# Optimization experiments

Measured on AMD Instinct MI355X. Metric: run time of the kernel, lower is better.

The kernel has to match this reference:

```python
import jax, jax.numpy as jnp
import numpy as np

N, IN_DIM, L, K, D = 131072, 128, 16, 8, 50
ENC_H, DEC_H, HEAD_H, DF = 64, 16, 64, 1.0


def setup_inputs() -> dict:
    key = jax.random.key(0)
    ks = jax.random.split(key, 20)
    s = lambda k, shape, fan: jax.random.normal(k, shape, jnp.float32) * (1.0 / np.sqrt(fan))
    return {
        "x": jax.random.normal(ks[0], (N, IN_DIM), jnp.float32),
        # encoder: in -> 64 -> 64 -> L
        "We1": s(ks[1], (IN_DIM, ENC_H), IN_DIM), "be1": jnp.zeros((ENC_H,), jnp.float32),
        "We2": s(ks[2], (ENC_H, ENC_H), ENC_H),   "be2": jnp.zeros((ENC_H,), jnp.float32),
        "We3": s(ks[3], (ENC_H, L), ENC_H),       "be3": jnp.zeros((L,), jnp.float32),
        # decoder: L -> 16 -> in
        "Wd1": s(ks[4], (L, DEC_H), L),           "bd1": jnp.zeros((DEC_H,), jnp.float32),
        "Wd2": s(ks[5], (DEC_H, IN_DIM), DEC_H),  "bd2": jnp.zeros((IN_DIM,), jnp.float32),
        # K per-cluster survival heads: (L+in) -> 64 -> num_durations
        "Wh1": s(ks[6], (K, L + IN_DIM, HEAD_H), L + IN_DIM), "bh1": jnp.zeros((K, HEAD_H), jnp.float32),
        "Wh2": s(ks[7], (K, HEAD_H, D), HEAD_H),              "bh2": jnp.zeros((K, D), jnp.float32),
        # cluster centers buffer
        "centers": jax.random.normal(ks[8], (K, L), jnp.float32) * 0.05,
    }


def _student_t_sim(z, centers, df):
    # z: [N, L], centers: [K, L] -> q: [N, K]
    dist2 = jnp.sum((z[:, None, :] - centers[None, :, :]) ** 2, axis=-1)
    logits = -0.5 * (df + 1.0) * jnp.log1p(dist2 / df)
    return jax.nn.softmax(logits, axis=1)


def reference(x, We1, be1, We2, be2, We3, be3, Wd1, bd1, Wd2, bd2,
              Wh1, bh1, Wh2, bh2, centers):
    relu = jax.nn.relu
    # encoder (eval mode: dropout off, non-variational)
    e = relu(x @ We1 + be1)
    e = relu(e @ We2 + be2)
    z = e @ We3 + be3                      # [N, L]
    q = _student_t_sim(z, centers, DF)     # [N, K]
    h = jnp.concatenate([z, x], axis=1)    # [N, L+in]
    # cluster-argmax routing to per-cluster heads: compute all K, select winner
    cluster_idx = jnp.argmax(q, axis=1)    # [N]
    h1 = relu(jnp.einsum("nf,kfh->nkh", h, Wh1) + bh1[None])   # [N, K, H]
    lg = jnp.einsum("nkh,khd->nkd", h1, Wh2) + bh2[None]       # [N, K, D]
    surv_logits = jnp.take_along_axis(lg, cluster_idx[:, None, None], axis=1)[:, 0]  # [N, D]
    # decoder + reconstruction loss per sample
    d = relu(z @ Wd1 + bd1)
    x_hat = d @ Wd2 + bd2                  # [N, in]
    rec_ps = jnp.mean((x_hat - x) ** 2, axis=1)
    kld = jnp.zeros((x.shape[0],), x.dtype)
    return z, q, surv_logits, x_hat, rec_ps, kld
```

## Files before the change

### kernel.cpp

```cpp
#include <hip/hip_runtime.h>

#define NS 131072
#define KC 8
typedef unsigned long long u64;

#define LD4(P) (*reinterpret_cast<const float4*>(&sm[(P)]))
#define LD2(P) (*reinterpret_cast<const float2*>(&sm[(P)]))
#define ST4(P) (*reinterpret_cast<float4*>(&sm[(P)]))
#define ST2(P) (*reinterpret_cast<float2*>(&sm[(P)]))

#define FMA8(ACCR, AV, W0, W1) do { \
  ACCR[0]=fmaf((AV),(W0).x,ACCR[0]); ACCR[1]=fmaf((AV),(W0).y,ACCR[1]); \
  ACCR[2]=fmaf((AV),(W0).z,ACCR[2]); ACCR[3]=fmaf((AV),(W0).w,ACCR[3]); \
  ACCR[4]=fmaf((AV),(W1).x,ACCR[4]); ACCR[5]=fmaf((AV),(W1).y,ACCR[5]); \
  ACCR[6]=fmaf((AV),(W1).z,ACCR[6]); ACCR[7]=fmaf((AV),(W1).w,ACCR[7]); } while(0)

#define K4(ACC, ABASE, ASTR, AK, BBASE, BSTR, JOFF, BK) do { \
  const float4 b00=LD4((BBASE)+((BK)*4+0)*(BSTR)+(JOFF)), b01=LD4((BBASE)+((BK)*4+0)*(BSTR)+(JOFF)+4); \
  const float4 b10=LD4((BBASE)+((BK)*4+1)*(BSTR)+(JOFF)), b11=LD4((BBASE)+((BK)*4+1)*(BSTR)+(JOFF)+4); \
  const float4 b20=LD4((BBASE)+((BK)*4+2)*(BSTR)+(JOFF)), b21=LD4((BBASE)+((BK)*4+2)*(BSTR)+(JOFF)+4); \
  const float4 b30=LD4((BBASE)+((BK)*4+3)*(BSTR)+(JOFF)), b31=LD4((BBASE)+((BK)*4+3)*(BSTR)+(JOFF)+4); \
  _Pragma("unroll") \
  for (int m_ = 0; m_ < 8; ++m_) { \
    const float4 av = LD4((ABASE)+(st+32*m_)*(ASTR)+(AK)*4); \
    FMA8(ACC[m_], av.x, b00, b01); FMA8(ACC[m_], av.y, b10, b11); \
    FMA8(ACC[m_], av.z, b20, b21); FMA8(ACC[m_], av.w, b30, b31); } \
} while(0)

#define INIT88(ACC, BPTR, OFF) do { \
  const float4 u_ = *reinterpret_cast<const float4*>(&(BPTR)[(OFF)]); \
  const float4 v_ = *reinterpret_cast<const float4*>(&(BPTR)[(OFF)+4]); \
  _Pragma("unroll") for (int m_ = 0; m_ < 8; ++m_) { \
    ACC[m_][0]=u_.x; ACC[m_][1]=u_.y; ACC[m_][2]=u_.z; ACC[m_][3]=u_.w; \
    ACC[m_][4]=v_.x; ACC[m_][5]=v_.y; ACC[m_][6]=v_.z; ACC[m_][7]=v_.w; } \
} while(0)

#define RELU88(ACC) do { _Pragma("unroll") for (int m_=0;m_<8;++m_) \
  { _Pragma("unroll") for (int j_=0;j_<8;++j_) ACC[m_][j_]=fmaxf(ACC[m_][j_],0.f); } } while(0)

#define WRITE_E(ACC) do { _Pragma("unroll") for (int m_=0;m_<8;++m_){ \
  const int r_ = st + 32*m_; \
  ST4(AR + r_*72 + job)     = make_float4(ACC[m_][0],ACC[m_][1],ACC[m_][2],ACC[m_][3]); \
  ST4(AR + r_*72 + job + 4) = make_float4(ACC[m_][4],ACC[m_][5],ACC[m_][6],ACC[m_][7]); } } while(0)

#define AR  0
#define WB  18432
#define WD1 19520
#define SMW 19776

__global__ __launch_bounds__(256, 2) void k_enc(
    const float* __restrict__ x,
    const float* __restrict__ We1, const float* __restrict__ be1,
    const float* __restrict__ We2, const float* __restrict__ be2,
    const float* __restrict__ We3, const float* __restrict__ be3,
    const float* __restrict__ Wd1, const float* __restrict__ bd1,
    const float* __restrict__ Wd2, const float* __restrict__ bd2,
    const float* __restrict__ centers,
    float* __restrict__ out_z, float* __restrict__ out_q,
    float* __restrict__ xhat, float* __restrict__ rec, float* __restrict__ kld,
    int* __restrict__ cidx, int* __restrict__ counts)
{
    __shared__ float sm[SMW];
    const int t  = threadIdx.x;
    const int ot = t & 7, st = t >> 3;
    const int job = ot * 8;
    const int s0 = blockIdx.x * 256;

    {
        float acc1[8][8];
        INIT88(acc1, be1, job);
        #pragma unroll 1
        for (int c = 0; c < 8; ++c) {
            #pragma unroll
            for (int p = 0; p < 4; ++p) {
                const int g = p*256 + t, row = g >> 2, c4 = (g & 3) * 4;
                ST4(AR + row*20 + c4) = *reinterpret_cast<const float4*>(
                    &x[(size_t)(s0+row)*128 + c*16 + c4]);
            }
            {   const int row = t >> 4, c4 = (t & 15) * 4;
                ST4(WB + row*68 + c4) = *reinterpret_cast<const float4*>(
                    &We1[(size_t)(c*16 + row)*64 + c4]); }
            __syncthreads();
            #pragma unroll
            for (int kc = 0; kc < 4; ++kc) K4(acc1, AR, 20, kc, WB, 68, job, kc);
            __syncthreads();
        }
        RELU88(acc1);
        WRITE_E(acc1);
    }
    __syncthreads();

    {
        float acc2[8][8];
        INIT88(acc2, be2, job);
        #pragma unroll 1
        for (int c = 0; c < 4; ++c) {
            {   const int row = t >> 4, c4 = (t & 15) * 4;
                ST4(WB + row*68 + c4) = *reinterpret_cast<const float4*>(
                    &We2[(size_t)(c*16 + row)*64 + c4]); }
            __syncthreads();
            #pragma unroll
            for (int kc = 0; kc < 4; ++kc) K4(acc2, AR, 72, c*4 + kc, WB, 68, job, kc);
            __syncthreads();
        }
        RELU88(acc2);
        WRITE_E(acc2);
    }
    {   const int row = t >> 2, c4 = (t & 3) * 4;
        ST4(WB + row*16 + c4) = *reinterpret_cast<const float4*>(
            &We3[(size_t)row*16 + c4]); }
    if (t < 64) ST4(WD1 + (t >> 2)*16 + (t & 3)*4) =
        *reinterpret_cast<const float4*>(&Wd1[(t >> 2)*16 + (t & 3)*4]);
    __syncthreads();

    float zac[8][2];
    {   const float2 b3 = *reinterpret_cast<const float2*>(&be3[ot*2]);
        #pragma unroll
        for (int m = 0; m < 8; ++m) { zac[m][0] = b3.x; zac[m][1] = b3.y; } }
    #pragma unroll 2
    for (int kc = 0; kc < 16; ++kc) {
        const float2 w0 = LD2(WB + (kc*4+0)*16 + ot*2);
        const float2 w1 = LD2(WB + (kc*4+1)*16 + ot*2);
        const float2 w2 = LD2(WB + (kc*4+2)*16 + ot*2);
        const float2 w3 = LD2(WB + (kc*4+3)*16 + ot*2);
        #pragma unroll
        for (int m = 0; m < 8; ++m) {
            const float4 av = LD4(AR + (st + 32*m)*72 + kc*4);
            float sa = zac[m][0], sb = zac[m][1];
            sa = fmaf(av.x, w0.x, sa); sb = fmaf(av.x, w0.y, sb);
            sa = fmaf(av.y, w1.x, sa); sb = fmaf(av.y, w1.y, sb);
            sa = fmaf(av.z, w2.x, sa); sb = fmaf(av.z, w2.y, sb);
            sa = fmaf(av.w, w3.x, sa); sb = fmaf(av.w, w3.y, sb);
            zac[m][0] = sa; zac[m][1] = sb;
        }
    }
    #pragma unroll
    for (int m = 0; m < 8; ++m)
        *reinterpret_cast<float2*>(&out_z[(size_t)(s0 + st + 32*m)*16 + ot*2]) =
            make_float2(zac[m][0], zac[m][1]);
    __syncthreads();
    #pragma unroll
    for (int m = 0; m < 8; ++m)
        ST2(AR + (st + 32*m)*20 + ot*2) = make_float2(zac[m][0], zac[m][1]);
    {
        const int row = t >> 4, c4 = (t & 15) * 4;
        ST4(WB + row*68 + c4) = *reinterpret_cast<const float4*>(
            &Wd2[(size_t)row*128 + c4]); }
    __syncthreads();

    {
        const float4 z0 = LD4(AR + t*20 + 0), z1 = LD4(AR + t*20 + 4);
        const float4 z2 = LD4(AR + t*20 + 8), z3 = LD4(AR + t*20 + 12);
        const float zz[16] = {z0.x,z0.y,z0.z,z0.w, z1.x,z1.y,z1.z,z1.w,
                              z2.x,z2.y,z2.z,z2.w, z3.x,z3.y,z3.z,z3.w};
        float d2[KC];
        #pragma unroll
        for (int k = 0; k < KC; ++k) {
            float acc = 0.f;
            #pragma unroll
            for (int l = 0; l < 16; ++l) {
                const float dl = zz[l] - centers[k*16 + l];
                acc = fmaf(dl, dl, acc);
            }
            d2[k] = acc;
        }
        float lgt[KC], ex[KC];
        float mm = -1e30f;
        #pragma unroll
        for (int k = 0; k < KC; ++k) { lgt[k] = -log1pf(d2[k]); mm = fmaxf(mm, lgt[k]); }
        float ssum = 0.f;
        #pragma unroll
        for (int k = 0; k < KC; ++k) { ex[k] = expf(lgt[k] - mm); ssum += ex[k]; }
        const float inv = 1.f / ssum;
        float4* oq = reinterpret_cast<float4*>(&out_q[(size_t)(s0 + t)*8]);
        oq[0] = make_float4(ex[0]*inv, ex[1]*inv, ex[2]*inv, ex[3]*inv);
        oq[1] = make_float4(ex[4]*inv, ex[5]*inv, ex[6]*inv, ex[7]*inv);
        int ci = 0; float best = d2[0];
        #pragma unroll
        for (int k = 1; k < KC; ++k) if (d2[k] < best) { best = d2[k]; ci = k; }
        cidx[s0 + t] = ci;
        #pragma unroll
        for (int k = 0; k < KC; ++k) {
            const u64 mk = __ballot(ci == k);
            if ((t & 63) == 0 && mk) atomicAdd(&counts[k], (int)__popcll(mk));
        }
        kld[s0 + t] = 0.f;
    }

    {
        float dac[8][2];
        const float2 bb = *reinterpret_cast<const float2*>(&bd1[ot*2]);
        const float2 u0 = LD2(WD1 + 0*16 + ot*2),  u1 = LD2(WD1 + 1*16 + ot*2);
        const float2 u2 = LD2(WD1 + 2*16 + ot*2),  u3 = LD2(WD1 + 3*16 + ot*2);
        const float2 u4 = LD2(WD1 + 4*16 + ot*2),  u5 = LD2(WD1 + 5*16 + ot*2);
        const float2 u6 = LD2(WD1 + 6*16 + ot*2),  u7 = LD2(WD1 + 7*16 + ot*2);
        const float2 u8 = LD2(WD1 + 8*16 + ot*2),  u9 = LD2(WD1 + 9*16 + ot*2);
        const float2 uA = LD2(WD1 + 10*16 + ot*2), uB = LD2(WD1 + 11*16 + ot*2);
        const float2 uC = LD2(WD1 + 12*16 + ot*2), uD = LD2(WD1 + 13*16 + ot*2);
        const float2 uE = LD2(WD1 + 14*16 + ot*2), uF = LD2(WD1 + 15*16 + ot*2);
        #pragma unroll
        for (int m = 0; m < 8; ++m) {
            const int r = st + 32*m;
            const float4 a0 = LD4(AR + r*20 + 0), a1 = LD4(AR + r*20 + 4);
            const float4 a2 = LD4(AR + r*20 + 8), a3 = LD4(AR + r*20 + 12);
            float sa = bb.x, sb = bb.y;
            sa=fmaf(a0.x,u0.x,sa); sb=fmaf(a0.x,u0.y,sb);
            sa=fmaf(a0.y,u1.x,sa); sb=fmaf(a0.y,u1.y,sb);
            sa=fmaf(a0.z,u2.x,sa); sb=fmaf(a0.z,u2.y,sb);
            sa=fmaf(a0.w,u3.x,sa); sb=fmaf(a0.w,u3.y,sb);
            sa=fmaf(a1.x,u4.x,sa); sb=fmaf(a1.x,u4.y,sb);
            sa=fmaf(a1.y,u5.x,sa); sb=fmaf(a1.y,u5.y,sb);
            sa=fmaf(a1.z,u6.x,sa); sb=fmaf(a1.z,u6.y,sb);
            sa=fmaf(a1.w,u7.x,sa); sb=fmaf(a1.w,u7.y,sb);
            sa=fmaf(a2.x,u8.x,sa); sb=fmaf(a2.x,u8.y,sb);
            sa=fmaf(a2.y,u9.x,sa); sb=fmaf(a2.y,u9.y,sb);
            sa=fmaf(a2.z,uA.x,sa); sb=fmaf(a2.z,uA.y,sb);
            sa=fmaf(a2.w,uB.x,sa); sb=fmaf(a2.w,uB.y,sb);
            sa=fmaf(a3.x,uC.x,sa); sb=fmaf(a3.x,uC.y,sb);
            sa=fmaf(a3.y,uD.x,sa); sb=fmaf(a3.y,uD.y,sb);
            sa=fmaf(a3.z,uE.x,sa); sb=fmaf(a3.z,uE.y,sb);
            sa=fmaf(a3.w,uF.x,sa); sb=fmaf(a3.w,uF.y,sb);
            dac[m][0] = fmaxf(sa, 0.f); dac[m][1] = fmaxf(sb, 0.f);
        }
        __syncthreads();
        #pragma unroll
        for (int m = 0; m < 8; ++m)
            ST2(AR + (st + 32*m)*20 + ot*2) = make_float2(dac[m][0], dac[m][1]);
    }
    __syncthreads();

    float rp[8] = {0.f,0.f,0.f,0.f,0.f,0.f,0.f,0.f};
    {
        float accx[8][8];
        INIT88(accx, bd2, job);
        #pragma unroll
        for (int kc = 0; kc < 4; ++kc) K4(accx, AR, 20, kc, WB, 68, job, kc);
        #pragma unroll
        for (int m = 0; m < 8; ++m) {
            const int r = st + 32*m;
            const float4 xa = *reinterpret_cast<const float4*>(&x[(size_t)(s0+r)*128 + job]);
            const float4 xb = *reinterpret_cast<const float4*>(&x[(size_t)(s0+r)*128 + job + 4]);
            float df;
            df=accx[m][0]-xa.x; rp[m]=fmaf(df,df,rp[m]);
            df=accx[m][1]-xa.y; rp[m]=fmaf(df,df,rp[m]);
            df=accx[m][2]-xa.z; rp[m]=fmaf(df,df,rp[m]);
            df=accx[m][3]-xa.w; rp[m]=fmaf(df,df,rp[m]);
            df=accx[m][4]-xb.x; rp[m]=fmaf(df,df,rp[m]);
            df=accx[m][5]-xb.y; rp[m]=fmaf(df,df,rp[m]);
            df=accx[m][6]-xb.z; rp[m]=fmaf(df,df,rp[m]);
            df=accx[m][7]-xb.w; rp[m]=fmaf(df,df,rp[m]);
            float4* o = reinterpret_cast<float4*>(&xhat[(size_t)(s0+r)*128 + job]);
            o[0] = make_float4(accx[m][0],accx[m][1],accx[m][2],accx[m][3]);
            o[1] = make_float4(accx[m][4],accx[m][5],accx[m][6],accx[m][7]);
        }
    }
    __syncthreads();
    {   const int row = t >> 4, c4 = (t & 15) * 4;
        ST4(WB + row*68 + c4) = *reinterpret_cast<const float4*>(
            &Wd2[(size_t)row*128 + 64 + c4]); }
    __syncthreads();
    {
        float accx[8][8];
        INIT88(accx, bd2, 64 + job);
        #pragma unroll
        for (int kc = 0; kc < 4; ++kc) K4(accx, AR, 20, kc, WB, 68, job, kc);
        #pragma unroll
        for (int m = 0; m < 8; ++m) {
            const int r = st + 32*m;
            const float4 xa = *reinterpret_cast<const float4*>(&x[(size_t)(s0+r)*128 + 64 + job]);
            const float4 xb = *reinterpret_cast<const float4*>(&x[(size_t)(s0+r)*128 + 64 + job + 4]);
            float df;
            df=accx[m][0]-xa.x; rp[m]=fmaf(df,df,rp[m]);
            df=accx[m][1]-xa.y; rp[m]=fmaf(df,df,rp[m]);
            df=accx[m][2]-xa.z; rp[m]=fmaf(df,df,rp[m]);
            df=accx[m][3]-xa.w; rp[m]=fmaf(df,df,rp[m]);
            df=accx[m][4]-xb.x; rp[m]=fmaf(df,df,rp[m]);
            df=accx[m][5]-xb.y; rp[m]=fmaf(df,df,rp[m]);
            df=accx[m][6]-xb.z; rp[m]=fmaf(df,df,rp[m]);
            df=accx[m][7]-xb.w; rp[m]=fmaf(df,df,rp[m]);
            float4* o = reinterpret_cast<float4*>(&xhat[(size_t)(s0+r)*128 + 64 + job]);
            o[0] = make_float4(accx[m][0],accx[m][1],accx[m][2],accx[m][3]);
            o[1] = make_float4(accx[m][4],accx[m][5],accx[m][6],accx[m][7]);
        }
    }
    #pragma unroll
    for (int m = 0; m < 8; ++m) {
        float v = rp[m];
        v += __shfl_xor(v, 1); v += __shfl_xor(v, 2); v += __shfl_xor(v, 4);
        if (ot == 0) rec[s0 + st + 32*m] = v * (1.f/128.f);
    }
}

__global__ void k_scan(const int* __restrict__ counts,
                       int* __restrict__ bases, int* __restrict__ cursors)
{
    if (threadIdx.x == 0) {
        int acc = 0;
        for (int k = 0; k < KC; ++k) { bases[k] = acc; cursors[k] = acc; acc += counts[k]; }
    }
}

__global__ __launch_bounds__(256) void k_scatter(
    const int* __restrict__ cidx, int* __restrict__ cursors, int* __restrict__ seg)
{
    const int s = blockIdx.x * 256 + threadIdx.x;
    const int lane = threadIdx.x & 63;
    const int ci = cidx[s];
    #pragma unroll
    for (int k = 0; k < KC; ++k) {
        const u64 mk = __ballot(ci == k);
        if (ci == k) {
            const int leader = __ffsll(mk) - 1;
            int base = 0;
            if (lane == leader) base = atomicAdd(&cursors[k], (int)__popcll(mk));
            base = __shfl(base, leader, 64);
            seg[base + (int)__popcll(mk & (((u64)1 << lane) - 1))] = s;
        }
    }
}

#define SMH 19520

__global__ __launch_bounds__(256, 2) void k_heads(
    const float* __restrict__ x, const float* __restrict__ zread,
    const float* __restrict__ Wh1, const float* __restrict__ bh1,
    const float* __restrict__ Wh2, const float* __restrict__ bh2,
    const int* __restrict__ counts, const int* __restrict__ bases,
    const int* __restrict__ seg,
    float* __restrict__ surv)
{
    __shared__ float sm[SMH];
    __shared__ int idxs[256];
    const int t  = threadIdx.x;
    const int ot = t & 7, st = t >> 3;
    const int job = ot * 8;

    int kk = -1, chunk = 0, pref = 0;
    #pragma unroll
    for (int q = 0; q < KC; ++q) {
        const int ck = (counts[q] + 255) >> 8;
        if (kk < 0) {
            if ((int)blockIdx.x < pref + ck) { kk = q; chunk = (int)blockIdx.x - pref; }
            pref += ck;
        }
    }
    if (kk < 0) return;
    kk    = __builtin_amdgcn_readfirstlane(kk);
    chunk = __builtin_amdgcn_readfirstlane(chunk);
    const int cnt  = __builtin_amdgcn_readfirstlane(counts[kk]);
    const int base = __builtin_amdgcn_readfirstlane(bases[kk]);

    {   const int i = chunk*256 + t;
        idxs[t] = seg[base + ((i < cnt) ? i : (cnt - 1))]; }
    __syncthreads();

    {
        float acc1[8][8];
        INIT88(acc1, bh1, (size_t)kk*64 + job);
        #pragma unroll
        for (int p = 0; p < 4; ++p) {
            const int g = p*256 + t, row = g >> 2, c4 = (g & 3) * 4;
            ST4(AR + row*20 + c4) = *reinterpret_cast<const float4*>(
                &zread[(size_t)idxs[row]*16 + c4]);
        }
        {   const int row = t >> 4, c4 = (t & 15) * 4;
            ST4(WB + row*68 + c4) = *reinterpret_cast<const float4*>(
                &Wh1[((size_t)kk*144 + row)*64 + c4]); }
        __syncthreads();
        #pragma unroll
        for (int kc = 0; kc < 4; ++kc) K4(acc1, AR, 20, kc, WB, 68, job, kc);
        __syncthreads();
        #pragma unroll 1
        for (int c = 0; c < 8; ++c) {
            #pragma unroll
            for (int p = 0; p < 4; ++p) {
                const int g = p*256 + t, row = g >> 2, c4 = (g & 3) * 4;
                ST4(AR + row*20 + c4) = *reinterpret_cast<const float4*>(
                    &x[(size_t)idxs[row]*128 + c*16 + c4]);
            }
            {   const int row = t >> 4, c4 = (t & 15) * 4;
                ST4(WB + row*68 + c4) = *reinterpret_cast<const float4*>(
                    &Wh1[((size_t)kk*144 + 16 + c*16 + row)*64 + c4]); }
            __syncthreads();
            #pragma unroll
            for (int kc = 0; kc < 4; ++kc) K4(acc1, AR, 20, kc, WB, 68, job, kc);
            __syncthreads();
        }
        RELU88(acc1);
        WRITE_E(acc1);
    }
    __syncthreads();

    float acc2[8][8];
    {   float bz[8];
        #pragma unroll
        for (int j = 0; j < 8; ++j) {
            const int col = job + j;
            bz[j] = (col < 50) ? bh2[(size_t)kk*50 + col] : 0.f;
        }
        #pragma unroll
        for (int m = 0; m < 8; ++m) {
            #pragma unroll
            for (int j = 0; j < 8; ++j) acc2[m][j] = bz[j];
        } }
    #pragma unroll 1
    for (int c = 0; c < 4; ++c) {
        {   const int row = t >> 4, c0 = (t & 15) * 4;
            const int gk = c*16 + row;
            float4 v;
            v.x = (c0+0 < 50) ? Wh2[((size_t)kk*64 + gk)*50 + c0+0] : 0.f;
            v.y = (c0+1 < 50) ? Wh2[((size_t)kk*64 + gk)*50 + c0+1] : 0.f;
            v.z = (c0+2 < 50) ? Wh2[((size_t)kk*64 + gk)*50 + c0+2] : 0.f;
            v.w = (c0+3 < 50) ? Wh2[((size_t)kk*64 + gk)*50 + c0+3] : 0.f;
            ST4(WB + row*68 + c0) = v; }
        __syncthreads();
        #pragma unroll
        for (int kc = 0; kc < 4; ++kc) K4(acc2, AR, 72, c*4 + kc, WB, 68, job, kc);
        __syncthreads();
    }

    #pragma unroll
    for (int m = 0; m < 8; ++m) {
        const int r = st + 32*m;
        if (chunk*256 + r < cnt) {
            float* so = &surv[(size_t)idxs[r]*50 + job];
            if (ot < 6) {
                *reinterpret_cast<float2*>(&so[0]) = make_float2(acc2[m][0], acc2[m][1]);
                *reinterpret_cast<float2*>(&so[2]) = make_float2(acc2[m][2], acc2[m][3]);
                *reinterpret_cast<float2*>(&so[4]) = make_float2(acc2[m][4], acc2[m][5]);
                *reinterpret_cast<float2*>(&so[6]) = make_float2(acc2[m][6], acc2[m][7]);
            } else if (ot == 6) {
                *reinterpret_cast<float2*>(&so[0]) = make_float2(acc2[m][0], acc2[m][1]);
            }
        }
    }
}

extern "C" void kernel_launch(void* const* d_in, const int* in_sizes, int n_in,
                              void* d_out, int out_size, void* d_ws, size_t ws_size,
                              hipStream_t stream)
{
    const float* x   = (const float*)d_in[0];
    const float* We1 = (const float*)d_in[1];
    const float* be1 = (const float*)d_in[2];
    const float* We2 = (const float*)d_in[3];
    const float* be2 = (const float*)d_in[4];
    const float* We3 = (const float*)d_in[5];
    const float* be3 = (const float*)d_in[6];
    const float* Wd1 = (const float*)d_in[7];
    const float* bd1 = (const float*)d_in[8];
    const float* Wd2 = (const float*)d_in[9];
    const float* bd2 = (const float*)d_in[10];
    const float* Wh1 = (const float*)d_in[11];
    const float* bh1 = (const float*)d_in[12];
    const float* Wh2 = (const float*)d_in[13];
    const float* bh2 = (const float*)d_in[14];
    const float* cen = (const float*)d_in[15];
    float* out = (float*)d_out;

    float* out_z  = out;
    float* out_q  = out + (size_t)NS * 16;
    float* out_sv = out + (size_t)NS * 24;
    float* out_xh = out + (size_t)NS * 74;
    float* out_rc = out + (size_t)NS * 202;
    float* out_kl = out + (size_t)NS * 203;

    int* cidx    = (int*)d_ws;
    int* counts  = cidx + NS;
    int* bases   = counts + KC;
    int* cursors = bases + KC;
    int* seg     = cursors + KC;

    hipMemsetAsync(counts, 0, KC * sizeof(int), stream);

    k_enc<<<dim3(NS / 256), dim3(256), 0, stream>>>(
        x, We1, be1, We2, be2, We3, be3, Wd1, bd1, Wd2, bd2, cen,
        out_z, out_q, out_xh, out_rc, out_kl, cidx, counts);

    k_scan<<<dim3(1), dim3(64), 0, stream>>>(counts, bases, cursors);

    k_scatter<<<dim3(NS / 256), dim3(256), 0, stream>>>(cidx, cursors, seg);

    k_heads<<<dim3(NS / 256 + KC), dim3(256), 0, stream>>>(
        x, out_z, Wh1, bh1, Wh2, bh2, counts, bases, seg, out_sv);
}
```

Baseline: 497.3 us.

## Prefetch next x/weight chunks into registers during FMA loops

The encoder and head GEMM loops now load the next chunk of x and the weights into registers before computing on the current chunk, so global load latency overlaps the FMAs instead of stalling behind a barrier. The activation row stride in shared memory drops from 72 to 68 floats, which shrinks the LDS footprint. Launch bounds change from 2 to 1 blocks per SM, allowing more registers per thread to hold the prefetch buffers. The risk is lower occupancy, which could expose latency elsewhere, and a possible change in LDS bank conflicts from the new stride.

Result: no change. 501.6 us (+0.9%).

```diff
diff --git a/kernel.cpp b/kernel.cpp
--- a/kernel.cpp
+++ b/kernel.cpp
@@ -8,6 +8,7 @@
 #define LD2(P) (*reinterpret_cast<const float2*>(&sm[(P)]))
 #define ST4(P) (*reinterpret_cast<float4*>(&sm[(P)]))
 #define ST2(P) (*reinterpret_cast<float2*>(&sm[(P)]))
+#define GL4(P) (*reinterpret_cast<const float4*>(&(P)))
 
 #define FMA8(ACCR, AV, W0, W1) do { \
   ACCR[0]=fmaf((AV),(W0).x,ACCR[0]); ACCR[1]=fmaf((AV),(W0).y,ACCR[1]); \
@@ -40,15 +41,21 @@
 
 #define WRITE_E(ACC) do { _Pragma("unroll") for (int m_=0;m_<8;++m_){ \
   const int r_ = st + 32*m_; \
-  ST4(AR + r_*72 + job)     = make_float4(ACC[m_][0],ACC[m_][1],ACC[m_][2],ACC[m_][3]); \
-  ST4(AR + r_*72 + job + 4) = make_float4(ACC[m_][4],ACC[m_][5],ACC[m_][6],ACC[m_][7]); } } while(0)
+  ST4(AR + r_*68 + job)     = make_float4(ACC[m_][0],ACC[m_][1],ACC[m_][2],ACC[m_][3]); \
+  ST4(AR + r_*68 + job + 4) = make_float4(ACC[m_][4],ACC[m_][5],ACC[m_][6],ACC[m_][7]); } } while(0)
+
+#define STAGE_X() do { \
+  ST4(AR + (xr0      )*20 + xc) = rx0; \
+  ST4(AR + (xr0 +  64)*20 + xc) = rx1; \
+  ST4(AR + (xr0 + 128)*20 + xc) = rx2; \
+  ST4(AR + (xr0 + 192)*20 + xc) = rx3; } while(0)
 
 #define AR  0
-#define WB  18432
-#define WD1 19520
-#define SMW 19776
-
-__global__ __launch_bounds__(256, 2) void k_enc(
+#define WB  17408
+#define WD1 18496
+#define SMW 18752
+
+__global__ __launch_bounds__(256, 1) void k_enc(
     const float* __restrict__ x,
     const float* __restrict__ We1, const float* __restrict__ be1,
     const float* __restrict__ We2, const float* __restrict__ be2,
@@ -65,52 +72,59 @@
     const int ot = t & 7, st = t >> 3;
     const int job = ot * 8;
     const int s0 = blockIdx.x * 256;
+    const int xr0 = t >> 2, xc = (t & 3) * 4;
+    const int wr  = t >> 4, wc = (t & 15) * 4;
 
     {
         float acc1[8][8];
         INIT88(acc1, be1, job);
+        float4 rx0 = GL4(x[(size_t)(s0+xr0      )*128 + xc]);
+        float4 rx1 = GL4(x[(size_t)(s0+xr0 +  64)*128 + xc]);
+        float4 rx2 = GL4(x[(size_t)(s0+xr0 + 128)*128 + xc]);
+        float4 rx3 = GL4(x[(size_t)(s0+xr0 + 192)*128 + xc]);
+        float4 rw  = GL4(We1[(size_t)wr*64 + wc]);
         #pragma unroll 1
         for (int c = 0; c < 8; ++c) {
-            #pragma unroll
-            for (int p = 0; p < 4; ++p) {
-                const int g = p*256 + t, row = g >> 2, c4 = (g & 3) * 4;
-                ST4(AR + row*20 + c4) = *reinterpret_cast<const float4*>(
-                    &x[(size_t)(s0+row)*128 + c*16 + c4]);
+            __syncthreads();
+            STAGE_X();
+            ST4(WB + wr*68 + wc) = rw;
+            __syncthreads();
+            if (c < 7) {
+                rx0 = GL4(x[(size_t)(s0+xr0      )*128 + (c+1)*16 + xc]);
+                rx1 = GL4(x[(size_t)(s0+xr0 +  64)*128 + (c+1)*16 + xc]);
+                rx2 = GL4(x[(size_t)(s0+xr0 + 128)*128 + (c+1)*16 + xc]);
+                rx3 = GL4(x[(size_t)(s0+xr0 + 192)*128 + (c+1)*16 + xc]);
+                rw  = GL4(We1[(size_t)((c+1)*16 + wr)*64 + wc]);
             }
-            {   const int row = t >> 4, c4 = (t & 15) * 4;
-                ST4(WB + row*68 + c4) = *reinterpret_cast<const float4*>(
-                    &We1[(size_t)(c*16 + row)*64 + c4]); }
-            __syncthreads();
             #pragma unroll
             for (int kc = 0; kc < 4; ++kc) K4(acc1, AR, 20, kc, WB, 68, job, kc);
-            __syncthreads();
-        }
+        }
+        __syncthreads();
         RELU88(acc1);
         WRITE_E(acc1);
     }
-    __syncthreads();
 
     {
         float acc2[8][8];
         INIT88(acc2, be2, job);
+        float4 rw = GL4(We2[(size_t)wr*64 + wc]);
         #pragma unroll 1
         for (int c = 0; c < 4; ++c) {
-            {   const int row = t >> 4, c4 = (t & 15) * 4;
-                ST4(WB + row*68 + c4) = *reinterpret_cast<const float4*>(
-                    &We2[(size_t)(c*16 + row)*64 + c4]); }
             __syncthreads();
+            ST4(WB + wr*68 + wc) = rw;
+            __syncthreads();
+            if (c < 3) rw = GL4(We2[(size_t)((c+1)*16 + wr)*64 + wc]);
             #pragma unroll
-            for (int kc = 0; kc < 4; ++kc) K4(acc2, AR, 72, c*4 + kc, WB, 68, job, kc);
-            __syncthreads();
-        }
+            for (int kc = 0; kc < 4; ++kc) K4(acc2, AR, 68, c*4 + kc, WB, 68, job, kc);
+        }
+        __syncthreads();
         RELU88(acc2);
         WRITE_E(acc2);
     }
     {   const int row = t >> 2, c4 = (t & 3) * 4;
-        ST4(WB + row*16 + c4) = *reinterpret_cast<const float4*>(
-            &We3[(size_t)row*16 + c4]); }
+        ST4(WB + row*16 + c4) = GL4(We3[(size_t)row*16 + c4]); }
     if (t < 64) ST4(WD1 + (t >> 2)*16 + (t & 3)*4) =
-        *reinterpret_cast<const float4*>(&Wd1[(t >> 2)*16 + (t & 3)*4]);
+        GL4(Wd1[(t >> 2)*16 + (t & 3)*4]);
     __syncthreads();
 
     float zac[8][2];
@@ -125,7 +139,7 @@
         const float2 w3 = LD2(WB + (kc*4+3)*16 + ot*2);
         #pragma unroll
         for (int m = 0; m < 8; ++m) {
-            const float4 av = LD4(AR + (st + 32*m)*72 + kc*4);
+            const float4 av = LD4(AR + (st + 32*m)*68 + kc*4);
             float sa = zac[m][0], sb = zac[m][1];
             sa = fmaf(av.x, w0.x, sa); sb = fmaf(av.x, w0.y, sb);
             sa = fmaf(av.y, w1.x, sa); sb = fmaf(av.y, w1.y, sb);
@@ -143,9 +157,7 @@
     for (int m = 0; m < 8; ++m)
         ST2(AR + (st + 32*m)*20 + ot*2) = make_float2(zac[m][0], zac[m][1]);
     {
-        const int row = t >> 4, c4 = (t & 15) * 4;
-        ST4(WB + row*68 + c4) = *reinterpret_cast<const float4*>(
-            &Wd2[(size_t)row*128 + c4]); }
+        ST4(WB + wr*68 + wc) = GL4(Wd2[(size_t)wr*128 + wc]); }
     __syncthreads();
 
     {
@@ -230,6 +242,7 @@
     __syncthreads();
 
     float rp[8] = {0.f,0.f,0.f,0.f,0.f,0.f,0.f,0.f};
+    float4 rw2 = GL4(Wd2[(size_t)wr*128 + 64 + wc]);
     {
         float accx[8][8];
         INIT88(accx, bd2, job);
@@ -238,8 +251,8 @@
         #pragma unroll
         for (int m = 0; m < 8; ++m) {
             const int r = st + 32*m;
-            const float4 xa = *reinterpret_cast<const float4*>(&x[(size_t)(s0+r)*128 + job]);
-            const float4 xb = *reinterpret_cast<const float4*>(&x[(size_t)(s0+r)*128 + job + 4]);
+            const float4 xa = GL4(x[(size_t)(s0+r)*128 + job]);
+            const float4 xb = GL4(x[(size_t)(s0+r)*128 + job + 4]);
             float df;
             df=accx[m][0]-xa.x; rp[m]=fmaf(df,df,rp[m]);
             df=accx[m][1]-xa.y; rp[m]=fmaf(df,df,rp[m]);
@@ -255,9 +268,7 @@
         }
     }
     __syncthreads();
-    {   const int row = t >> 4, c4 = (t & 15) * 4;
-        ST4(WB + row*68 + c4) = *reinterpret_cast<const float4*>(
-            &Wd2[(size_t)row*128 + 64 + c4]); }
+    ST4(WB + wr*68 + wc) = rw2;
     __syncthreads();
     {
         float accx[8][8];
@@ -267,8 +278,8 @@
         #pragma unroll
         for (int m = 0; m < 8; ++m) {
             const int r = st + 32*m;
-            const float4 xa = *reinterpret_cast<const float4*>(&x[(size_t)(s0+r)*128 + 64 + job]);
-            const float4 xb = *reinterpret_cast<const float4*>(&x[(size_t)(s0+r)*128 + 64 + job + 4]);
+            const float4 xa = GL4(x[(size_t)(s0+r)*128 + 64 + job]);
+            const float4 xb = GL4(x[(size_t)(s0+r)*128 + 64 + job + 4]);
             float df;
             df=accx[m][0]-xa.x; rp[m]=fmaf(df,df,rp[m]);
             df=accx[m][1]-xa.y; rp[m]=fmaf(df,df,rp[m]);
@@ -319,9 +330,9 @@
     }
 }
 
-#define SMH 19520
-
-__global__ __launch_bounds__(256, 2) void k_heads(
+#define SMH 18496
+
+__global__ __launch_bounds__(256, 1) void k_heads(
     const float* __restrict__ x, const float* __restrict__ zread,
     const float* __restrict__ Wh1, const float* __restrict__ bh1,
     const float* __restrict__ Wh2, const float* __restrict__ bh2,
@@ -334,6 +345,8 @@
     const int t  = threadIdx.x;
     const int ot = t & 7, st = t >> 3;
     const int job = ot * 8;
+    const int xr0 = t >> 2, xc = (t & 3) * 4;
+    const int wr  = t >> 4, wc = (t & 15) * 4;
 
     int kk = -1, chunk = 0, pref = 0;
     #pragma unroll
@@ -353,43 +366,45 @@
     {   const int i = chunk*256 + t;
         idxs[t] = seg[base + ((i < cnt) ? i : (cnt - 1))]; }
     __syncthreads();
+    const int i0 = idxs[xr0], i1 = idxs[xr0+64], i2 = idxs[xr0+128], i3 = idxs[xr0+192];
 
     {
         float acc1[8][8];
         INIT88(acc1, bh1, (size_t)kk*64 + job);
-        #pragma unroll
-        for (int p = 0; p < 4; ++p) {
-            const int g = p*256 + t, row = g >> 2, c4 = (g & 3) * 4;
-            ST4(AR + row*20 + c4) = *reinterpret_cast<const float4*>(
-                &zread[(size_t)idxs[row]*16 + c4]);
-        }
-        {   const int row = t >> 4, c4 = (t & 15) * 4;
-            ST4(WB + row*68 + c4) = *reinterpret_cast<const float4*>(
-                &Wh1[((size_t)kk*144 + row)*64 + c4]); }
-        __syncthreads();
+        {   const int zc = (t & 3) * 4;
+            ST4(AR + (xr0      )*20 + zc) = GL4(zread[(size_t)i0*16 + zc]);
+            ST4(AR + (xr0 +  64)*20 + zc) = GL4(zread[(size_t)i1*16 + zc]);
+            ST4(AR + (xr0 + 128)*20 + zc) = GL4(zread[(size_t)i2*16 + zc]);
+            ST4(AR + (xr0 + 192)*20 + zc) = GL4(zread[(size_t)i3*16 + zc]);
+            ST4(WB + wr*68 + wc) = GL4(Wh1[((size_t)kk*144 + wr)*64 + wc]); }
+        __syncthreads();
+        float4 rx0 = GL4(x[(size_t)i0*128 + xc]);
+        float4 rx1 = GL4(x[(size_t)i1*128 + xc]);
+        float4 rx2 = GL4(x[(size_t)i2*128 + xc]);
+        float4 rx3 = GL4(x[(size_t)i3*128 + xc]);
+        float4 rw  = GL4(Wh1[((size_t)kk*144 + 16 + wr)*64 + wc]);
         #pragma unroll
         for (int kc = 0; kc < 4; ++kc) K4(acc1, AR, 20, kc, WB, 68, job, kc);
-        __syncthreads();
         #pragma unroll 1
         for (int c = 0; c < 8; ++c) {
-            #pragma unroll
-            for (int p = 0; p < 4; ++p) {
-                const int g = p*256 + t, row = g >> 2, c4 = (g & 3) * 4;
-                ST4(AR + row*20 + c4) = *reinterpret_cast<const float4*>(
-                    &x[(size_t)idxs[row]*128 + c*16 + c4]);
+            __syncthreads();
+            STAGE_X();
+            ST4(WB + wr*68 + wc) = rw;
+            __syncthreads();
+            if (c < 7) {
+                rx0 = GL4(x[(size_t)i0*128 + (c+1)*16 + xc]);
+                rx1 = GL4(x[(size_t)i1*128 + (c+1)*16 + xc]);
+                rx2 = GL4(x[(size_t)i2*128 + (c+1)*16 + xc]);
+                rx3 = GL4(x[(size_t)i3*128 + (c+1)*16 + xc]);
+                rw  = GL4(Wh1[((size_t)kk*144 + 16 + (c+1)*16 + wr)*64 + wc]);
             }
-            {   const int row = t >> 4, c4 = (t & 15) * 4;
-                ST4(WB + row*68 + c4) = *reinterpret_cast<const float4*>(
-                    &Wh1[((size_t)kk*144 + 16 + c*16 + row)*64 + c4]); }
-            __syncthreads();
             #pragma unroll
             for (int kc = 0; kc < 4; ++kc) K4(acc1, AR, 20, kc, WB, 68, job, kc);
-            __syncthreads();
-        }
+        }
+        __syncthreads();
         RELU88(acc1);
         WRITE_E(acc1);
     }
-    __syncthreads();
 
     float acc2[8][8];
     {   float bz[8];
@@ -403,20 +418,26 @@
             #pragma unroll
             for (int j = 0; j < 8; ++j) acc2[m][j] = bz[j];
         } }
+    float4 rv;
+    {   const int gk = wr;
+        rv.x = (wc+0 < 50) ? Wh2[((size_t)kk*64 + gk)*50 + wc+0] : 0.f;
+        rv.y = (wc+1 < 50) ? Wh2[((size_t)kk*64 + gk)*50 + wc+1] : 0.f;
+        rv.z = (wc+2 < 50) ? Wh2[((size_t)kk*64 + gk)*50 + wc+2] : 0.f;
+        rv.w = (wc+3 < 50) ? Wh2[((size_t)kk*64 + gk)*50 + wc+3] : 0.f; }
     #pragma unroll 1
     for (int c = 0; c < 4; ++c) {
-        {   const int row = t >> 4, c0 = (t & 15) * 4;
-            const int gk = c*16 + row;
-            float4 v;
-            v.x = (c0+0 < 50) ? Wh2[((size_t)kk*64 + gk)*50 + c0+0] : 0.f;
-            v.y = (c0+1 < 50) ? Wh2[((size_t)kk*64 + gk)*50 + c0+1] : 0.f;
-            v.z = (c0+2 < 50) ? Wh2[((size_t)kk*64 + gk)*50 + c0+2] : 0.f;
-            v.w = (c0+3 < 50) ? Wh2[((size_t)kk*64 + gk)*50 + c0+3] : 0.f;
-            ST4(WB + row*68 + c0) = v; }
-        __syncthreads();
-        #pragma unroll
-        for (int kc = 0; kc < 4; ++kc) K4(acc2, AR, 72, c*4 + kc, WB, 68, job, kc);
-        __syncthreads();
+        __syncthreads();
+        ST4(WB + wr*68 + wc) = rv;
+        __syncthreads();
+        if (c < 3) {
+            const int gk = (c+1)*16 + wr;
+            rv.x = (wc+0 < 50) ? Wh2[((size_t)kk*64 + gk)*50 + wc+0] : 0.f;
+            rv.y = (wc+1 < 50) ? Wh2[((size_t)kk*64 + gk)*50 + wc+1] : 0.f;
+            rv.z = (wc+2 < 50) ? Wh2[((size_t)kk*64 + gk)*50 + wc+2] : 0.f;
+            rv.w = (wc+3 < 50) ? Wh2[((size_t)kk*64 + gk)*50 + wc+3] : 0.f;
+        }
+        #pragma unroll
+        for (int kc = 0; kc < 4; ++kc) K4(acc2, AR, 68, c*4 + kc, WB, 68, job, kc);
     }
 
     #pragma unroll
```
